# Kernel optimization log

Measured on AMD Instinct MI355X. Metric: run time of the kernel, lower is better.

## Reference

```python
import jax, jax.numpy as jnp
import numpy as np

B, T, D, H = 4, 1024, 1024, 16
HD = D // H
DFF = 2048          # ExpertTier hidden width
K = 3               # ConvTier causal kernel size
NEG = -1e9


def layernorm(x, w, b, eps=1e-5):
    m = jnp.mean(x, axis=-1, keepdims=True)
    v = jnp.var(x, axis=-1, keepdims=True)
    return (x - m) * jax.lax.rsqrt(v + eps) * w + b


def rope_cos_sin(t, hd):
    inv = 1.0 / (10000.0 ** (jnp.arange(0, hd, 2, dtype=jnp.float32) / hd))
    freqs = jnp.outer(jnp.arange(t, dtype=jnp.float32), inv)  # (T, hd/2)
    return jnp.cos(freqs), jnp.sin(freqs)


def apply_rope(x, cos, sin):
    # x: (B, H, T, hd); cos/sin: (T, hd/2)
    x1, x2 = jnp.split(x, 2, axis=-1)
    return jnp.concatenate([x1 * cos - x2 * sin, x1 * sin + x2 * cos], axis=-1)


def causal_attn(q, k, v):
    # q,k,v: (..., T, d); full causal softmax attention
    t = q.shape[-2]
    scale = 1.0 / jnp.sqrt(jnp.asarray(q.shape[-1], q.dtype))
    scores = jnp.einsum('...qd,...kd->...qk', q, k) * scale
    mask = jnp.triu(jnp.ones((t, t), dtype=bool), k=1)
    scores = jnp.where(mask, NEG, scores)
    w = jax.nn.softmax(scores, axis=-1)
    return jnp.einsum('...qk,...kd->...qd', w, v)


def setup_inputs() -> dict:
    key = jax.random.key(0)
    ks = jax.random.split(key, 16)
    ws = 0.02
    g = lambda k, shape, s: jax.random.normal(k, shape, dtype=jnp.float32) * s
    return {
        'x': g(ks[0], (B, T, D), 1.0),
        'ln1_w': jnp.ones((D,), jnp.float32), 'ln1_b': jnp.zeros((D,), jnp.float32),
        'qkv_w': g(ks[1], (D, 3 * D), ws),
        'out_w': g(ks[2], (D, D), ws),
        'ln2_w': jnp.ones((D,), jnp.float32), 'ln2_b': jnp.zeros((D,), jnp.float32),
        'router_w': g(ks[3], (D, 4), ws),
        'conv_w': g(ks[4], (D, 1, K), 0.1),             # depthwise OIW, groups=D
        'expert_w1': g(ks[5], (D, DFF), ws),
        'expert_w2': g(ks[6], (DFF, D), ws),
        'at_wq': g(ks[7], (D, D), ws),
        'at_wk': g(ks[8], (D, D), ws),
        'at_wv': g(ks[9], (D, D), ws),
        'at_wo': g(ks[10], (D, D), ws),
        'tier_gate': jnp.full((D,), 0.1, jnp.float32),
        'sink_kv_scale': jnp.asarray(0.1, jnp.float32),
    }


def reference(x, ln1_w, ln1_b, qkv_w, out_w, ln2_w, ln2_b, router_w, conv_w,
              expert_w1, expert_w2, at_wq, at_wk, at_wv, at_wo,
              tier_gate, sink_kv_scale):
    b, t, d = x.shape
    # --- backbone causal self-attention with RoPE (pre-norm) ---
    h1 = layernorm(x, ln1_w, ln1_b)
    qkv = (h1 @ qkv_w).reshape(b, t, 3, H, HD)
    q = qkv[:, :, 0].transpose(0, 2, 1, 3)  # (B,H,T,hd)
    k = qkv[:, :, 1].transpose(0, 2, 1, 3)
    v = qkv[:, :, 2].transpose(0, 2, 1, 3)
    cos, sin = rope_cos_sin(t, HD)
    q = apply_rope(q, cos, sin)
    k = apply_rope(k, cos, sin)
    ao = causal_attn(q, k, v)                         # (B,H,T,hd)
    ao = ao.transpose(0, 2, 1, 3).reshape(b, t, d) @ out_w
    x = x + ao
    # --- router + tiers ---
    h = layernorm(x, ln2_w, ln2_b)
    routing_w = jax.nn.softmax(h @ router_w, axis=-1)  # (B,T,4): conv/expert/attn/sink
    # ConvTier: depthwise causal conv (k=3) + GELU
    hc = jnp.pad(h.transpose(0, 2, 1), ((0, 0), (0, 0), (K - 1, 0)))  # (B,D,T+K-1)
    conv = jax.lax.conv_general_dilated(hc, conv_w, (1,), 'VALID',
                                        feature_group_count=d,
                                        dimension_numbers=('NCH', 'OIH', 'NCH'))
    conv_out = jax.nn.gelu(conv.transpose(0, 2, 1))   # (B,T,D)
    # ExpertTier: 2-layer GELU MLP
    expert_out = jax.nn.gelu(h @ expert_w1) @ expert_w2
    # AttentionTier: single-head causal attention
    attn2 = causal_attn(h @ at_wq, h @ at_wk, h @ at_wv) @ at_wo
    # SinkTier outputs zeros -> contributes nothing to the weighted sum
    combined = (conv_out * routing_w[..., 0:1]
                + expert_out * routing_w[..., 1:2]
                + attn2 * routing_w[..., 2:3])
    x = x + combined * tier_gate
    # sink kv scaling
    kv_scale = 1.0 - routing_w[..., 3] * (1.0 - jnp.abs(sink_kv_scale))
    x = x * kv_scale[..., None]
    return (x, routing_w)
```

## Files before the change

kernel.cpp:

```cpp
#include <hip/hip_runtime.h>

#define Bz 4
#define Tz 1024
#define Dz 1024
#define Hz 16
#define NTz (Bz*Tz)

typedef short s8v __attribute__((ext_vector_type(8)));
typedef float f4v __attribute__((ext_vector_type(4)));

__device__ __forceinline__ float bf2f(unsigned short u){
  unsigned int x = ((unsigned int)u) << 16;
  return __builtin_bit_cast(float, x);
}
__device__ __forceinline__ unsigned short f2bf(float f){
  unsigned int x = __builtin_bit_cast(unsigned int, f);
  x += 0x7fffu + ((x >> 16) & 1u);
  return (unsigned short)(x >> 16);
}
__device__ __forceinline__ float gelu_f(float x){
  float z = 1.5957691216057308f * (x + 0.044715f * x * x * x);
  return x / (1.0f + __expf(-z));
}
__device__ __forceinline__ void gl16(const unsigned short* g, unsigned short* l){
  __builtin_amdgcn_global_load_lds(
      (const __attribute__((address_space(1))) unsigned int*)g,
      (__attribute__((address_space(3))) unsigned int*)l, 16, 0, 0);
}

struct WSeg { const float* in; unsigned short* out; int R, C, blk0, bx; };
struct WPack { WSeg s[8]; };
__global__ __launch_bounds__(256) void k_convtrans_all(WPack p)
{
  __shared__ float tile[32][33];
  int bid = blockIdx.x;
  const float* in = p.s[0].in; unsigned short* out = p.s[0].out;
  int R = p.s[0].R, C = p.s[0].C, blk0 = 0, bx = p.s[0].bx;
  #pragma unroll
  for (int i = 1; i < 8; ++i) {
    if (bid >= p.s[i].blk0) {
      in = p.s[i].in; out = p.s[i].out; R = p.s[i].R; C = p.s[i].C;
      blk0 = p.s[i].blk0; bx = p.s[i].bx;
    }
  }
  int rel = bid - blk0;
  int c0 = (rel % bx) * 32, r0 = (rel / bx) * 32;
  int tx = threadIdx.x & 31, ty = threadIdx.x >> 5;
  #pragma unroll
  for (int i = 0; i < 32; i += 8)
    tile[ty + i][tx] = in[(long)(r0 + ty + i) * C + c0 + tx];
  __syncthreads();
  #pragma unroll
  for (int i = 0; i < 32; i += 8)
    out[(long)(c0 + ty + i) * R + r0 + tx] = f2bf(tile[tx][ty + i]);
}

__global__ __launch_bounds__(256) void k_convtrans_b(const unsigned short* __restrict__ in,
    unsigned short* __restrict__ out, int ld, long sIn, long sOut)
{
  __shared__ unsigned short tile[32][34];
  in  += (long)blockIdx.z * sIn;
  out += (long)blockIdx.z * sOut;
  int c0 = blockIdx.x * 32, r0 = blockIdx.y * 32;
  int tx = threadIdx.x & 31, ty = threadIdx.x >> 5;
  #pragma unroll
  for (int i = 0; i < 32; i += 8)
    tile[ty + i][tx] = in[(long)(r0 + ty + i) * ld + c0 + tx];
  __syncthreads();
  #pragma unroll
  for (int i = 0; i < 32; i += 8)
    out[(long)(c0 + ty + i) * 1024 + r0 + tx] = tile[tx][ty + i];
}

__global__ __launch_bounds__(256) void k_layernorm(const float* __restrict__ x,
    const float* __restrict__ w, const float* __restrict__ b,
    unsigned short* __restrict__ out)
{
  int row = blockIdx.x, tid = threadIdx.x;
  const float4* xp = (const float4*)(x + (long)row * Dz);
  float4 v = xp[tid];
  float s  = v.x + v.y + v.z + v.w;
  float ss = v.x*v.x + v.y*v.y + v.z*v.z + v.w*v.w;
  int lane = tid & 63, wv = tid >> 6;
  #pragma unroll
  for (int off = 32; off; off >>= 1){ s += __shfl_xor(s, off); ss += __shfl_xor(ss, off); }
  __shared__ float red[8];
  if (lane == 0){ red[wv] = s; red[4 + wv] = ss; }
  __syncthreads();
  s  = red[0] + red[1] + red[2] + red[3];
  ss = red[4] + red[5] + red[6] + red[7];
  float mean = s * (1.0f / Dz);
  float var  = ss * (1.0f / Dz) - mean * mean;
  float rstd = rsqrtf(var + 1e-5f);
  float4 wg = ((const float4*)w)[tid];
  float4 bg = ((const float4*)b)[tid];
  ushort4 ov;
  ov.x = f2bf((v.x - mean) * rstd * wg.x + bg.x);
  ov.y = f2bf((v.y - mean) * rstd * wg.y + bg.y);
  ov.z = f2bf((v.z - mean) * rstd * wg.z + bg.z);
  ov.w = f2bf((v.w - mean) * rstd * wg.w + bg.w);
  *((ushort4*)(out + (long)row * Dz) + tid) = ov;
}

__global__ __launch_bounds__(256) void k_ln_router(const unsigned short* __restrict__ x2,
    const float* __restrict__ w, const float* __restrict__ b,
    const float* __restrict__ rw, unsigned short* __restrict__ out,
    float* __restrict__ rout)
{
  int row = blockIdx.x, tid = threadIdx.x;
  ushort4 xu = *((const ushort4*)(x2 + (long)row * Dz) + tid);
  float4 v = {bf2f(xu.x), bf2f(xu.y), bf2f(xu.z), bf2f(xu.w)};
  float s  = v.x + v.y + v.z + v.w;
  float ss = v.x*v.x + v.y*v.y + v.z*v.z + v.w*v.w;
  int lane = tid & 63, wv = tid >> 6;
  #pragma unroll
  for (int off = 32; off; off >>= 1){ s += __shfl_xor(s, off); ss += __shfl_xor(ss, off); }
  __shared__ float red[8];
  if (lane == 0){ red[wv] = s; red[4 + wv] = ss; }
  __syncthreads();
  s  = red[0] + red[1] + red[2] + red[3];
  ss = red[4] + red[5] + red[6] + red[7];
  float mean = s * (1.0f / Dz);
  float var  = ss * (1.0f / Dz) - mean * mean;
  float rstd = rsqrtf(var + 1e-5f);
  float4 wg = ((const float4*)w)[tid];
  float4 bg = ((const float4*)b)[tid];
  float h0 = (v.x - mean) * rstd * wg.x + bg.x;
  float h1 = (v.y - mean) * rstd * wg.y + bg.y;
  float h2 = (v.z - mean) * rstd * wg.z + bg.z;
  float h3 = (v.w - mean) * rstd * wg.w + bg.w;
  ushort4 ov;
  ov.x = f2bf(h0); ov.y = f2bf(h1); ov.z = f2bf(h2); ov.w = f2bf(h3);
  *((ushort4*)(out + (long)row * Dz) + tid) = ov;
  int d0 = tid * 4;
  float4 r0 = *(const float4*)(rw + (long)d0 * 4);
  float4 r1 = *(const float4*)(rw + (long)(d0 + 1) * 4);
  float4 r2 = *(const float4*)(rw + (long)(d0 + 2) * 4);
  float4 r3 = *(const float4*)(rw + (long)(d0 + 3) * 4);
  float a0 = h0*r0.x + h1*r1.x + h2*r2.x + h3*r3.x;
  float a1 = h0*r0.y + h1*r1.y + h2*r2.y + h3*r3.y;
  float a2 = h0*r0.z + h1*r1.z + h2*r2.z + h3*r3.z;
  float a3 = h0*r0.w + h1*r1.w + h2*r2.w + h3*r3.w;
  #pragma unroll
  for (int off = 32; off; off >>= 1) {
    a0 += __shfl_xor(a0, off); a1 += __shfl_xor(a1, off);
    a2 += __shfl_xor(a2, off); a3 += __shfl_xor(a3, off);
  }
  __shared__ float red2[4][4];
  if (lane == 0){ red2[wv][0] = a0; red2[wv][1] = a1; red2[wv][2] = a2; red2[wv][3] = a3; }
  __syncthreads();
  if (tid == 0) {
    float s0 = red2[0][0] + red2[1][0] + red2[2][0] + red2[3][0];
    float s1 = red2[0][1] + red2[1][1] + red2[2][1] + red2[3][1];
    float s2 = red2[0][2] + red2[1][2] + red2[2][2] + red2[3][2];
    float s3 = red2[0][3] + red2[1][3] + red2[2][3] + red2[3][3];
    float mx = fmaxf(fmaxf(s0, s1), fmaxf(s2, s3));
    float e0 = __expf(s0 - mx), e1 = __expf(s1 - mx);
    float e2 = __expf(s2 - mx), e3 = __expf(s3 - mx);
    float inv = 1.0f / (e0 + e1 + e2 + e3);
    float4 r = {e0 * inv, e1 * inv, e2 * inv, e3 * inv};
    *(float4*)(rout + (long)row * 4) = r;
  }
}

template<int MODE, int BN, bool TRIMAP, bool TRIK, bool DBUF>
__global__ __launch_bounds__(256) void k_gemm(
    const unsigned short* __restrict__ A,
    const unsigned short* __restrict__ Bt,
    float* __restrict__ Cf, unsigned short* __restrict__ Cb,
    const float* __restrict__ addsrc,
    unsigned short* __restrict__ P1, unsigned short* __restrict__ P2,
    int N, int K, int lda, int ldb,
    long sA, long sB, long sC)
{
  constexpr int BM = 128;
  constexpr int MREP = (BN == 128) ? 4 : 2;
  constexpr int NB = DBUF ? 2 : 1;
  __shared__ unsigned short As[NB][BM * 64];
  __shared__ unsigned short Bs[NB][BN * 64];
  int bm, bn;
  if (TRIMAP) {
    int li = blockIdx.x;
    int nwg = gridDim.x;
    if ((nwg & 7) == 0) li = (li & 7) * (nwg >> 3) + (li >> 3);
    int r = (int)((sqrtf(4.f * li + 1.f) - 1.f) * 0.5f);
    if ((r + 1) * (r + 2) <= li) ++r;
    if (r * (r + 1) > li) --r;
    bm = r * 128; bn = (li - r * (r + 1)) * BN;
  } else {
    int lin = blockIdx.y * gridDim.x + blockIdx.x;
    int nwg = gridDim.x * gridDim.y;
    if ((nwg & 7) == 0) lin = (lin & 7) * (nwg >> 3) + (lin >> 3);
    int cols = gridDim.x, rows = gridDim.y;
    constexpr int GM = 8;
    int in_grp = GM * cols;
    int gid = lin / in_grp;
    int fm = gid * GM;
    int gsz = min(rows - fm, GM);
    int rem = lin - gid * in_grp;
    int pm = fm + (rem % gsz);
    int pn = rem / gsz;
    if (TRIK) pm = rows - 1 - pm;
    bm = pm * BM; bn = pn * BN;
  }
  A  += (long)blockIdx.z * sA;
  Bt += (long)blockIdx.z * sB;
  int tid = threadIdx.x, w = tid >> 6, lane = tid & 63;
  int wr, wc;
  if (BN == 128) { wr = (w >> 1) * 64; wc = (w & 1) * 64; }
  else           { wr = w * 32;        wc = 0; }
  f4v acc[MREP][4];
  #pragma unroll
  for (int m = 0; m < MREP; ++m)
    #pragma unroll
    for (int n = 0; n < 4; ++n)
      acc[m][n] = (f4v){0.f, 0.f, 0.f, 0.f};

  int Keff = K;
  if (TRIK) Keff = min(K, bm + BM);

  int lrow = lane >> 3;
  int lcol = (((lane & 7) ^ lrow) * 8);
  const unsigned short* AgJ[4];
  int AsOff[4];
  #pragma unroll
  for (int j = 0; j < 4; ++j) {
    AgJ[j] = A + (long)(bm + w * 32 + j * 8 + lrow) * lda + lcol;
    AsOff[j] = (w * 32 + j * 8) * 64;
  }
  constexpr int BCH = BN / 8 / 4;
  const unsigned short* BgJ[BCH];
  int BsOff[BCH];
  #pragma unroll
  for (int j = 0; j < BCH; ++j) {
    BgJ[j] = Bt + (long)(bn + w * (BCH * 8) + j * 8 + lrow) * ldb + lcol;
    BsOff[j] = (w * (BCH * 8) + j * 8) * 64;
  }

  int fr = lane & 15, fg = lane >> 4;
  int sw = (fr & 7) * 8;

  auto stage = [&](int buf, int k0){
    #pragma unroll
    for (int j = 0; j < 4; ++j) gl16(AgJ[j] + k0, &As[buf][AsOff[j]]);
    #pragma unroll
    for (int j = 0; j < BCH; ++j) gl16(BgJ[j] + k0, &Bs[buf][BsOff[j]]);
  };
  auto compute = [&](int buf){
    #pragma unroll
    for (int kk = 0; kk < 2; ++kk) {
      int kg = (kk * 32 + fg * 8) ^ sw;
      s8v af[MREP], bfv[4];
      #pragma unroll
      for (int m = 0; m < MREP; ++m) af[m]  = *(const s8v*)&As[buf][(wr + m * 16 + fr) * 64 + kg];
      #pragma unroll
      for (int n = 0; n < 4; ++n)    bfv[n] = *(const s8v*)&Bs[buf][(wc + n * 16 + fr) * 64 + kg];
      #pragma unroll
      for (int m = 0; m < MREP; ++m)
        #pragma unroll
        for (int n = 0; n < 4; ++n)
          acc[m][n] = __builtin_amdgcn_mfma_f32_16x16x32_bf16(af[m], bfv[n], acc[m][n], 0, 0, 0);
    }
  };

  if (DBUF) {
    int cur = 0;
    stage(0, 0);
    __syncthreads();
    for (int k0 = 0; k0 < Keff; k0 += 64) {
      if (k0 + 64 < Keff) stage(cur ^ 1, k0 + 64);
      compute(cur);
      __syncthreads();
      cur ^= 1;
    }
  } else {
    for (int k0 = 0; k0 < Keff; k0 += 64) {
      __syncthreads();
      stage(0, k0);
      __syncthreads();
      compute(0);
    }
  }

  int cr0 = bm + wr + fg * 4;
  int cc0 = bn + wc + fr;

  if (MODE == 4) {
    int sect = bn >> 10;
    if (sect == 2) {
      #pragma unroll
      for (int m = 0; m < MREP; ++m)
        #pragma unroll
        for (int n = 0; n < 4; ++n)
          #pragma unroll
          for (int i = 0; i < 4; ++i) {
            int row = cr0 + m * 16 + i;
            int vcol = (bn - 2048) + wc + n * 16 + fr;
            P2[(long)row * 1024 + vcol] = f2bf(acc[m][n][i]);
          }
    } else {
      unsigned short* dst = (sect == 0) ? Cb : P1;
      float scl = (sect == 0) ? 0.125f : 1.0f;
      int head = ((bn & 1023) + wc) >> 6;
      float inv0 = exp2f(-(float)fr * 0.4152410118609203f);
      float inv1 = exp2f(-(float)(fr + 16) * 0.4152410118609203f);
      #pragma unroll
      for (int m = 0; m < MREP; ++m)
        #pragma unroll
        for (int i = 0; i < 4; ++i) {
          int row = cr0 + m * 16 + i;
          int t = row & 1023, bq = row >> 10;
          float a0 = (float)t * inv0, a1 = (float)t * inv1;
          float cs0 = __cosf(a0), sn0 = __sinf(a0);
          float cs1 = __cosf(a1), sn1 = __sinf(a1);
          float v0 = acc[m][0][i], v1 = acc[m][1][i];
          float v2 = acc[m][2][i], v3 = acc[m][3][i];
          long base = ((long)(bq * 16 + head)) * 65536 + (long)t * 64 + fr;
          dst[base]      = f2bf((v0 * cs0 - v2 * sn0) * scl);
          dst[base + 32] = f2bf((v0 * sn0 + v2 * cs0) * scl);
          dst[base + 16] = f2bf((v1 * cs1 - v3 * sn1) * scl);
          dst[base + 48] = f2bf((v1 * sn1 + v3 * cs1) * scl);
        }
    }
    return;
  }

  #pragma unroll
  for (int m = 0; m < MREP; ++m)
    #pragma unroll
    for (int n = 0; n < 4; ++n)
      #pragma unroll
      for (int i = 0; i < 4; ++i) {
        long row = cr0 + m * 16 + i, col = cc0 + n * 16;
        long idx = (long)blockIdx.z * sC + row * (long)N + col;
        float v = acc[m][n][i];
        if (MODE == 1 || MODE == 7) v += addsrc[idx];
        if (MODE == 5) { if (col < 2048) v = gelu_f(v); }
        if (MODE == 6) v *= 0.03125f;
        if (MODE <= 1) Cf[idx] = v; else Cb[idx] = f2bf(v);
      }
}

__global__ __launch_bounds__(256) void k_attn_mfma(
    const unsigned short* __restrict__ Qb, const unsigned short* __restrict__ Kb,
    const unsigned short* __restrict__ Vt, unsigned short* __restrict__ ao)
{
  __shared__ unsigned short Ks[64][72];
  __shared__ unsigned short Vs[64][72];
  __shared__ unsigned short Ps[4][16][72];
  int qb = 15 - (blockIdx.x >> 6);
  int bh = blockIdx.x & 63;
  int b = bh >> 4, h = bh & 15;
  int t0 = qb * 64;
  int tid = threadIdx.x, w = tid >> 6, lane = tid & 63;
  int fr = lane & 15, fg = lane >> 4;

  const unsigned short* qp = Qb + (long)bh * Tz * 64 + (long)(t0 + w * 16 + fr) * 64 + fg * 8;
  s8v qf[2] = { *(const s8v*)qp, *(const s8v*)(qp + 32) };

  f4v o_acc[4];
  #pragma unroll
  for (int n = 0; n < 4; ++n) o_acc[n] = (f4v){0.f, 0.f, 0.f, 0.f};
  float m_[4] = {-1e30f, -1e30f, -1e30f, -1e30f};
  float l_[4] = {0.f, 0.f, 0.f, 0.f};

  int sr = tid >> 3, sc = (tid & 7) * 8;
  const unsigned short* Kg = Kb + (long)bh * Tz * 64 + (long)sr * 64 + sc;
  const unsigned short* Vg = Vt + (long)bh * 64 * Tz + (long)sr * Tz + sc;

  uint4 pk0, pk1, pv0, pv1;
  auto loadregs = [&](int k0){
    pk0 = *(const uint4*)(Kg + (long)k0 * 64);
    pk1 = *(const uint4*)(Kg + (long)(k0 + 32) * 64);
    pv0 = *(const uint4*)(Vg + k0);
    pv1 = *(const uint4*)(Vg + (long)32 * Tz + k0);
  };
  auto storelds = [&](){
    *(uint4*)&Ks[sr][sc]      = pk0;
    *(uint4*)&Ks[sr + 32][sc] = pk1;
    *(uint4*)&Vs[sr][sc]      = pv0;
    *(uint4*)&Vs[sr + 32][sc] = pv1;
  };

  loadregs(0);
  storelds();
  __syncthreads();

  for (int kt = 0; kt <= qb; ++kt) {
    int k0 = kt * 64;
    if (kt < qb) loadregs(k0 + 64);

    f4v sacc[4];
    #pragma unroll
    for (int n = 0; n < 4; ++n) sacc[n] = (f4v){0.f, 0.f, 0.f, 0.f};
    #pragma unroll
    for (int kk = 0; kk < 2; ++kk) {
      int kg = kk * 32 + fg * 8;
      #pragma unroll
      for (int n = 0; n < 4; ++n) {
        s8v bf = *(const s8v*)&Ks[n * 16 + fr][kg];
        sacc[n] = __builtin_amdgcn_mfma_f32_16x16x32_bf16(qf[kk], bf, sacc[n], 0, 0, 0);
      }
    }

    bool full = (kt < qb);
    float p[4][4], alpha[4];
    #pragma unroll
    for (int i = 0; i < 4; ++i) {
      int trow = t0 + w * 16 + fg * 4 + i;
      float mx = -1e30f;
      #pragma unroll
      for (int n = 0; n < 4; ++n) {
        float sval = sacc[n][i];
        if (!full) {
          int key = k0 + n * 16 + fr;
          sval = (key <= trow) ? sval : -1e30f;
        }
        p[n][i] = sval;
        mx = fmaxf(mx, sval);
      }
      mx = fmaxf(mx, __shfl_xor(mx, 1));
      mx = fmaxf(mx, __shfl_xor(mx, 2));
      mx = fmaxf(mx, __shfl_xor(mx, 4));
      mx = fmaxf(mx, __shfl_xor(mx, 8));
      float mnew = fmaxf(m_[i], mx);
      alpha[i] = __expf(m_[i] - mnew);
      m_[i] = mnew;
      float ps = 0.f;
      #pragma unroll
      for (int n = 0; n < 4; ++n) {
        float pv = __expf(p[n][i] - mnew);
        p[n][i] = pv;
        ps += pv;
      }
      ps += __shfl_xor(ps, 1); ps += __shfl_xor(ps, 2);
      ps += __shfl_xor(ps, 4); ps += __shfl_xor(ps, 8);
      l_[i] = l_[i] * alpha[i] + ps;
    }
    #pragma unroll
    for (int n = 0; n < 4; ++n)
      #pragma unroll
      for (int i = 0; i < 4; ++i)
        o_acc[n][i] *= alpha[i];
    #pragma unroll
    for (int n = 0; n < 4; ++n)
      #pragma unroll
      for (int i = 0; i < 4; ++i)
        Ps[w][fg * 4 + i][n * 16 + fr] = f2bf(p[n][i]);

    #pragma unroll
    for (int kk = 0; kk < 2; ++kk) {
      int kg = kk * 32 + fg * 8;
      s8v pa = *(const s8v*)&Ps[w][fr][kg];
      #pragma unroll
      for (int n = 0; n < 4; ++n) {
        s8v vb = *(const s8v*)&Vs[n * 16 + fr][kg];
        o_acc[n] = __builtin_amdgcn_mfma_f32_16x16x32_bf16(pa, vb, o_acc[n], 0, 0, 0);
      }
    }

    if (kt < qb) {
      __syncthreads();
      storelds();
      __syncthreads();
    }
  }

  float inv[4];
  #pragma unroll
  for (int i = 0; i < 4; ++i) inv[i] = 1.0f / l_[i];
  #pragma unroll
  for (int n = 0; n < 4; ++n)
    #pragma unroll
    for (int i = 0; i < 4; ++i) {
      int t = t0 + w * 16 + fg * 4 + i;
      ao[((long)(b * Tz + t)) * Dz + h * 64 + n * 16 + fr] = f2bf(o_acc[n][i] * inv[i]);
    }
}

__global__ __launch_bounds__(256) void k_softmax_causal(const unsigned short* __restrict__ S,
    unsigned short* __restrict__ P)
{
  long row = blockIdx.x;
  int t = (int)(row & (Tz - 1));
  int tid = threadIdx.x;
  const unsigned short* sp = S + row * Tz;
  ushort4 v = ((const ushort4*)sp)[tid];
  float vv[4];
  vv[0] = (tid*4 + 0 <= t) ? bf2f(v.x) : -1e30f;
  vv[1] = (tid*4 + 1 <= t) ? bf2f(v.y) : -1e30f;
  vv[2] = (tid*4 + 2 <= t) ? bf2f(v.z) : -1e30f;
  vv[3] = (tid*4 + 3 <= t) ? bf2f(v.w) : -1e30f;
  float mx = fmaxf(fmaxf(vv[0], vv[1]), fmaxf(vv[2], vv[3]));
  int lane = tid & 63, wv = tid >> 6;
  #pragma unroll
  for (int off = 32; off; off >>= 1) mx = fmaxf(mx, __shfl_xor(mx, off));
  __shared__ float red[8];
  if (lane == 0) red[wv] = mx;
  __syncthreads();
  mx = fmaxf(fmaxf(red[0], red[1]), fmaxf(red[2], red[3]));
  float p[4];
  float s = 0.f;
  #pragma unroll
  for (int i = 0; i < 4; ++i){ p[i] = __expf(vv[i] - mx); s += p[i]; }
  #pragma unroll
  for (int off = 32; off; off >>= 1) s += __shfl_xor(s, off);
  if (lane == 0) red[4 + wv] = s;
  __syncthreads();
  s = red[4] + red[5] + red[6] + red[7];
  float inv = 1.0f / s;
  ushort4 ov;
  ov.x = f2bf(p[0] * inv); ov.y = f2bf(p[1] * inv);
  ov.z = f2bf(p[2] * inv); ov.w = f2bf(p[3] * inv);
  *((ushort4*)(P + row * Tz) + tid) = ov;
}

__global__ __launch_bounds__(256) void k_combine(
    const unsigned short* __restrict__ x2, const unsigned short* __restrict__ hbf,
    const unsigned short* __restrict__ eoa, const unsigned short* __restrict__ eob,
    const unsigned short* __restrict__ ap,
    const float* __restrict__ rout, const float* __restrict__ convw,
    const float* __restrict__ tg, const float* __restrict__ sinkp,
    float* __restrict__ outx)
{
  int row = blockIdx.x, tid = threadIdx.x;
  int t = row & (Tz - 1), b = row >> 10;
  int d0 = tid * 4;
  ushort4 xu = *(const ushort4*)(x2 + (long)row * Dz + d0);
  ushort4 ea = *(const ushort4*)(eoa + (long)row * Dz + d0);
  ushort4 eb = *(const ushort4*)(eob + (long)row * Dz + d0);
  ushort4 a4 = *(const ushort4*)(ap + (long)row * Dz + d0);
  float4 t4 = *(const float4*)(tg + d0);
  float4 r4 = *(const float4*)(rout + (long)row * 4);
  float sks = fabsf(sinkp[0]);
  float kv = 1.0f - r4.w * (1.0f - sks);
  const float4* cwp = (const float4*)(convw + (long)d0 * 3);
  float4 c0 = cwp[0], c1 = cwp[1], c2 = cwp[2];
  float cwf[12] = {c0.x, c0.y, c0.z, c0.w, c1.x, c1.y, c1.z, c1.w, c2.x, c2.y, c2.z, c2.w};
  float hv[3][4];
  #pragma unroll
  for (int tap = 0; tap < 3; ++tap) {
    int tt = t - 2 + tap;
    if (tt >= 0) {
      ushort4 hu = *((const ushort4*)(hbf + ((long)(b * Tz + tt)) * Dz + d0));
      hv[tap][0] = bf2f(hu.x); hv[tap][1] = bf2f(hu.y);
      hv[tap][2] = bf2f(hu.z); hv[tap][3] = bf2f(hu.w);
    } else {
      hv[tap][0] = 0.f; hv[tap][1] = 0.f; hv[tap][2] = 0.f; hv[tap][3] = 0.f;
    }
  }
  float ov[4];
  float xi[4] = {bf2f(xu.x), bf2f(xu.y), bf2f(xu.z), bf2f(xu.w)};
  float ei[4] = {bf2f(ea.x) + bf2f(eb.x), bf2f(ea.y) + bf2f(eb.y),
                 bf2f(ea.z) + bf2f(eb.z), bf2f(ea.w) + bf2f(eb.w)};
  float ai[4] = {bf2f(a4.x), bf2f(a4.y), bf2f(a4.z), bf2f(a4.w)};
  float ti[4] = {t4.x, t4.y, t4.z, t4.w};
  #pragma unroll
  for (int i = 0; i < 4; ++i) {
    float conv = hv[0][i] * cwf[i*3 + 0] + hv[1][i] * cwf[i*3 + 1] + hv[2][i] * cwf[i*3 + 2];
    float comb = gelu_f(conv) * r4.x + ei[i] * r4.y + ai[i] * r4.z;
    ov[i] = (xi[i] + comb * ti[i]) * kv;
  }
  float4 res = {ov[0], ov[1], ov[2], ov[3]};
  *(float4*)(outx + (long)row * Dz + d0) = res;
}

extern "C" void kernel_launch(void* const* d_in, const int* in_sizes, int n_in,
                              void* d_out, int out_size, void* d_ws, size_t ws_size,
                              hipStream_t stream) {
  (void)in_sizes; (void)n_in; (void)out_size; (void)ws_size;
  const float* x       = (const float*)d_in[0];
  const float* ln1_w   = (const float*)d_in[1];
  const float* ln1_b   = (const float*)d_in[2];
  const float* qkv_w   = (const float*)d_in[3];
  const float* out_w   = (const float*)d_in[4];
  const float* ln2_w   = (const float*)d_in[5];
  const float* ln2_b   = (const float*)d_in[6];
  const float* router_w= (const float*)d_in[7];
  const float* conv_w  = (const float*)d_in[8];
  const float* ew1     = (const float*)d_in[9];
  const float* ew2     = (const float*)d_in[10];
  const float* at_wq   = (const float*)d_in[11];
  const float* at_wk   = (const float*)d_in[12];
  const float* at_wv   = (const float*)d_in[13];
  const float* at_wo   = (const float*)d_in[14];
  const float* tg      = (const float*)d_in[15];
  const float* sinkp   = (const float*)d_in[16];
  float* outx = (float*)d_out;
  float* rout = outx + (size_t)NTz * Dz;

  char* ws = (char*)d_ws;
  size_t off = 0;
  auto alloc = [&](size_t bytes) -> char* {
    char* p = ws + off;
    off += (bytes + 255) & ~(size_t)255;
    return p;
  };
  const long TD = (long)Tz * Dz, TT = (long)Tz * Tz;

  unsigned short* w_qkvt  = (unsigned short*)alloc((size_t)3072*1024*2);
  unsigned short* w_outt  = (unsigned short*)alloc((size_t)1024*1024*2);
  unsigned short* w_tiert = (unsigned short*)alloc((size_t)5120*1024*2);
  unsigned short* w_ew2t  = (unsigned short*)alloc((size_t)1024*2048*2);
  unsigned short* w_wot   = (unsigned short*)alloc((size_t)1024*1024*2);
  unsigned short* h1bf    = (unsigned short*)alloc((size_t)NTz*Dz*2);
  unsigned short* tierb   = (unsigned short*)alloc((size_t)NTz*5120*2);
  unsigned short* aobf    = (unsigned short*)alloc((size_t)NTz*Dz*2);
  unsigned short* x2b     = (unsigned short*)alloc((size_t)NTz*Dz*2);
  unsigned short* hbf     = (unsigned short*)alloc((size_t)NTz*Dz*2);
  unsigned short* Pbf     = (unsigned short*)alloc((size_t)Bz*Tz*Tz*2);
  unsigned short* v2tbf   = (unsigned short*)alloc((size_t)NTz*Dz*2);
  unsigned short* a2obf   = (unsigned short*)alloc((size_t)NTz*Dz*2);
  unsigned short* eofb    = (unsigned short*)alloc((size_t)NTz*Dz*2);
  unsigned short* a2pb    = (unsigned short*)alloc((size_t)NTz*Dz*2);
  unsigned short* Sbf     = (unsigned short*)alloc((size_t)Bz*Tz*Tz*2);

  unsigned short* Qb = x2b;
  unsigned short* Kb = Pbf;
  unsigned short* Vb = tierb;
  unsigned short* Vt = a2pb;
  unsigned short* eofb2 = h1bf;
  long eoDelta = (long)(eofb2 - eofb);

  dim3 blk(256);

  WPack wp;
  wp.s[0] = {qkv_w, w_qkvt,                         1024, 3072, 0,     96};
  wp.s[1] = {out_w, w_outt,                         1024, 1024, 3072,  32};
  wp.s[2] = {ew1,   w_tiert,                        1024, 2048, 4096,  64};
  wp.s[3] = {at_wq, w_tiert + 2048*1024,            1024, 1024, 6144,  32};
  wp.s[4] = {at_wk, w_tiert + 3072*1024,            1024, 1024, 7168,  32};
  wp.s[5] = {at_wv, w_tiert + (size_t)4096*1024,    1024, 1024, 8192,  32};
  wp.s[6] = {ew2,   w_ew2t,                         2048, 1024, 9216,  32};
  wp.s[7] = {at_wo, w_wot,                          1024, 1024, 11264, 32};
  k_convtrans_all<<<dim3(12288), blk, 0, stream>>>(wp);

  k_layernorm<<<NTz, blk, 0, stream>>>(x, ln1_w, ln1_b, h1bf);
  k_gemm<4,128,false,false,true><<<dim3(24, 32), blk, 0, stream>>>(h1bf, w_qkvt,
      nullptr, Qb, nullptr, Kb, Vb, 3072, 1024, 1024, 1024, 0, 0, 0);
  k_convtrans_b<<<dim3(32, 32, 4), blk, 0, stream>>>(Vb, Vt, 1024, TD, TD);
  k_attn_mfma<<<dim3(1024), blk, 0, stream>>>(Qb, Kb, Vt, aobf);
  k_gemm<7,64,false,false,true><<<dim3(16, 32), blk, 0, stream>>>(aobf, w_outt, nullptr,
      x2b, x, nullptr, nullptr, 1024, 1024, 1024, 1024, 0, 0, 0);
  k_ln_router<<<NTz, blk, 0, stream>>>(x2b, ln2_w, ln2_b, router_w, hbf, rout);
  k_gemm<5,128,false,false,true><<<dim3(40, 32), blk, 0, stream>>>(hbf, w_tiert,
      nullptr, tierb, nullptr, nullptr, nullptr, 5120, 1024, 1024, 1024, 0, 0, 0);
  k_gemm<3,64,false,false,true><<<dim3(16, 32, 2), blk, 0, stream>>>(tierb, w_ew2t,
      nullptr, eofb, nullptr, nullptr, nullptr, 1024, 1024, 5120, 2048,
      1024, 1024, eoDelta);
  k_convtrans_b<<<dim3(32, 32, 4), blk, 0, stream>>>(tierb + 4096, v2tbf, 5120,
      (long)Tz*5120, TD);
  k_gemm<6,64,true,false,true><<<dim3(72, 1, 4), blk, 0, stream>>>(tierb + 2048,
      tierb + 3072, nullptr, Sbf, nullptr, nullptr, nullptr,
      1024, 1024, 5120, 5120, (long)Tz*5120, (long)Tz*5120, TT);
  k_softmax_causal<<<NTz, blk, 0, stream>>>(Sbf, Pbf);
  k_gemm<3,64,false,true,true><<<dim3(16, 8, 4), blk, 0, stream>>>(Pbf, v2tbf, nullptr,
      a2obf, nullptr, nullptr, nullptr, 1024, 1024, 1024, 1024, TT, TD, TD);
  k_gemm<3,64,false,false,true><<<dim3(16, 32), blk, 0, stream>>>(a2obf, w_wot, nullptr,
      a2pb, nullptr, nullptr, nullptr, 1024, 1024, 1024, 1024, 0, 0, 0);
  k_combine<<<NTz, blk, 0, stream>>>(x2b, hbf, eofb, eofb2, a2pb, rout, conv_w,
      tg, sinkp, outx);
}
```

Baseline: 298.9 us.

## Add triple-buffered 64x128 GEMM for tier projection with grouped tile swizzle

Replaces the generic double-buffered 128x128 GEMM for the fused tier projection (expert W1 + attention Q/K/V, N=5120) with a dedicated kernel. The new kernel uses 64x128 tiles, three LDS stages with explicit vmcnt waits and barriers, and an XCD-aware grouped block remap that improves L2 reuse. The smaller tiles double the block count, giving more waves to fill the GPU and more loads in flight, at the cost of lower per-block data reuse. The MODE 5 GELU path is removed from the generic kernel and done only in the new one.

```diff
diff --git a/kernel.cpp b/kernel.cpp
--- a/kernel.cpp
+++ b/kernel.cpp
@@ -27,6 +27,9 @@
       (const __attribute__((address_space(1))) unsigned int*)g,
       (__attribute__((address_space(3))) unsigned int*)l, 16, 0, 0);
 }
+
+#define VM(n) asm volatile("s_waitcnt vmcnt(" #n ")" ::: "memory")
+#define BAR() asm volatile("s_barrier" ::: "memory")
 
 struct WSeg { const float* in; unsigned short* out; int R, C, blk0, bx; };
 struct WPack { WSeg s[8]; };
@@ -161,6 +164,107 @@
     float4 r = {e0 * inv, e1 * inv, e2 * inv, e3 * inv};
     *(float4*)(rout + (long)row * 4) = r;
   }
+}
+
+__global__ __launch_bounds__(256) void k_gemm3s(
+    const unsigned short* __restrict__ A,
+    const unsigned short* __restrict__ Bt,
+    unsigned short* __restrict__ Cb)
+{
+  constexpr int BM = 64, BN = 128, BK = 64;
+  __shared__ unsigned short As[3][BM * BK];
+  __shared__ unsigned short Bs[3][BN * BK];
+  int lin = blockIdx.y * gridDim.x + blockIdx.x;
+  int cols = gridDim.x, rows = gridDim.y;
+  int nwg = cols * rows;
+  if ((nwg & 7) == 0) lin = (lin & 7) * (nwg >> 3) + (lin >> 3);
+  int in_grp = 8 * cols;
+  int gid = lin / in_grp;
+  int fm = gid * 8;
+  int gsz = min(rows - fm, 8);
+  int rem = lin - gid * in_grp;
+  int pm = fm + (rem % gsz);
+  int pn = rem / gsz;
+  int bm = pm * BM, bn = pn * BN;
+
+  int tid = threadIdx.x, w = tid >> 6, lane = tid & 63;
+  int fr = lane & 15, fg = lane >> 4;
+  int sw = (fr & 7) * 8;
+  int wc = w * 32;
+  int lrow = lane >> 3;
+  int lcol = ((lane & 7) ^ lrow) * 8;
+
+  const unsigned short* AgJ[2];
+  int AsOff[2];
+  #pragma unroll
+  for (int j = 0; j < 2; ++j) {
+    AgJ[j] = A + (long)(bm + w * 16 + j * 8 + lrow) * 1024 + lcol;
+    AsOff[j] = (w * 16 + j * 8) * BK;
+  }
+  const unsigned short* BgJ[4];
+  int BsOff[4];
+  #pragma unroll
+  for (int j = 0; j < 4; ++j) {
+    BgJ[j] = Bt + (long)(bn + w * 32 + j * 8 + lrow) * 1024 + lcol;
+    BsOff[j] = (w * 32 + j * 8) * BK;
+  }
+
+  f4v acc[4][2];
+  #pragma unroll
+  for (int m = 0; m < 4; ++m)
+    #pragma unroll
+    for (int n = 0; n < 2; ++n)
+      acc[m][n] = (f4v){0.f, 0.f, 0.f, 0.f};
+
+  auto stage = [&](int buf, int kt){
+    int k0 = kt * BK;
+    #pragma unroll
+    for (int j = 0; j < 2; ++j) gl16(AgJ[j] + k0, &As[buf][AsOff[j]]);
+    #pragma unroll
+    for (int j = 0; j < 4; ++j) gl16(BgJ[j] + k0, &Bs[buf][BsOff[j]]);
+  };
+  auto compute = [&](int buf){
+    #pragma unroll
+    for (int kk = 0; kk < 2; ++kk) {
+      int kg = (kk * 32 + fg * 8) ^ sw;
+      s8v af[4], bfv[2];
+      #pragma unroll
+      for (int m = 0; m < 4; ++m) af[m]  = *(const s8v*)&As[buf][(m * 16 + fr) * BK + kg];
+      #pragma unroll
+      for (int n = 0; n < 2; ++n) bfv[n] = *(const s8v*)&Bs[buf][(wc + n * 16 + fr) * BK + kg];
+      #pragma unroll
+      for (int m = 0; m < 4; ++m)
+        #pragma unroll
+        for (int n = 0; n < 2; ++n)
+          acc[m][n] = __builtin_amdgcn_mfma_f32_16x16x32_bf16(af[m], bfv[n], acc[m][n], 0, 0, 0);
+    }
+  };
+
+  stage(0, 0);
+  stage(1, 1);
+  VM(6); BAR();
+  for (int k = 0; k < 14; ++k) {
+    stage((k + 2) % 3, k + 2);
+    VM(12); BAR();
+    compute(k % 3);
+    BAR();
+  }
+  VM(6); BAR(); compute(2); BAR();
+  VM(0); BAR(); compute(0);
+
+  int cr = bm + fg * 4, cc = bn + wc + fr;
+  #pragma unroll
+  for (int m = 0; m < 4; ++m)
+    #pragma unroll
+    for (int n = 0; n < 2; ++n)
+      #pragma unroll
+      for (int i = 0; i < 4; ++i) {
+        long row = cr + m * 16 + i;
+        long col = cc + n * 16;
+        float v = acc[m][n][i];
+        if (col < 2048) v = gelu_f(v);
+        Cb[row * 5120 + col] = f2bf(v);
+      }
 }
 
 template<int MODE, int BN, bool TRIMAP, bool TRIK, bool DBUF>
@@ -335,7 +439,6 @@
         long idx = (long)blockIdx.z * sC + row * (long)N + col;
         float v = acc[m][n][i];
         if (MODE == 1 || MODE == 7) v += addsrc[idx];
-        if (MODE == 5) { if (col < 2048) v = gelu_f(v); }
         if (MODE == 6) v *= 0.03125f;
         if (MODE <= 1) Cf[idx] = v; else Cb[idx] = f2bf(v);
       }
@@ -643,8 +746,7 @@
   k_gemm<7,64,false,false,true><<<dim3(16, 32), blk, 0, stream>>>(aobf, w_outt, nullptr,
       x2b, x, nullptr, nullptr, 1024, 1024, 1024, 1024, 0, 0, 0);
   k_ln_router<<<NTz, blk, 0, stream>>>(x2b, ln2_w, ln2_b, router_w, hbf, rout);
-  k_gemm<5,128,false,false,true><<<dim3(40, 32), blk, 0, stream>>>(hbf, w_tiert,
-      nullptr, tierb, nullptr, nullptr, nullptr, 5120, 1024, 1024, 1024, 0, 0, 0);
+  k_gemm3s<<<dim3(40, 64), blk, 0, stream>>>(hbf, w_tiert, tierb);
   k_gemm<3,64,false,false,true><<<dim3(16, 32, 2), blk, 0, stream>>>(tierb, w_ew2t,
       nullptr, eofb, nullptr, nullptr, nullptr, 1024, 1024, 5120, 2048,
       1024, 1024, eoDelta);
```

Result: no change. 302.5 us (+1.2%).
